# Kernel optimization log

Measured on AMD Instinct MI355X. Metric: run time of the kernel, lower is better.

## Reference

```python
import jax, jax.numpy as jnp
import numpy as np

EPS = 1e-12  # matches torch F.normalize eps


def _l2_normalize(v, axis):
    n = jnp.sqrt(jnp.sum(v * v, axis=axis, keepdims=True))
    return v / jnp.maximum(n, EPS)


def setup_inputs() -> dict:
    key = jax.random.key(0)
    k1, k2 = jax.random.split(key)
    N, D, K = 131072, 512, 64
    x = jax.random.normal(k1, (N, D), dtype=jnp.float32)
    clusters = jax.random.normal(k2, (K, D), dtype=jnp.float32)
    alpha = jnp.ones((), dtype=jnp.float32)
    return {"x": x, "clusters": clusters, "alpha": alpha}


def reference(x, clusters, alpha):
    # cosine similarity between normalized features and normalized codebook
    normed_clusters = _l2_normalize(clusters, axis=1)   # [K, D]
    normed_features = _l2_normalize(x, axis=-1)         # [N, D]
    inner_products = jnp.einsum('nd,kd->nk', normed_features, normed_clusters)  # [N, K]
    # alpha is not None branch: soft assignment
    cluster_probs = jax.nn.softmax(inner_products * alpha, axis=1)  # [N, K]
    cluster_loss = -jnp.mean(jnp.sum(cluster_probs * inner_products, axis=1))
    return cluster_loss, cluster_probs
```

## Files before the change

kernel.cpp:

```cpp
#include <hip/hip_runtime.h>
#include <hip/hip_bf16.h>

#define NROWS 131072
#define DIM   512
#define NK    64

typedef __attribute__((ext_vector_type(4))) float f32x4;
typedef __attribute__((ext_vector_type(8))) short s16x8;

static __device__ __forceinline__ unsigned pk2(float a, float b) {
    union { __hip_bfloat162 h; unsigned u; } cv;
    cv.h = __float22bfloat162_rn(make_float2(a, b));
    return cv.u;
}

__global__ void prep_kernel(const float* __restrict__ cl,
                            unsigned* __restrict__ cb,
                            float* __restrict__ loss_out) {
    const int k = blockIdx.x, t = threadIdx.x;
    const float4* rp = reinterpret_cast<const float4*>(cl + k * DIM);
    float4 f0 = rp[2 * t], f1 = rp[2 * t + 1];
    float ss = f0.x*f0.x + f0.y*f0.y + f0.z*f0.z + f0.w*f0.w
             + f1.x*f1.x + f1.y*f1.y + f1.z*f1.z + f1.w*f1.w;
#pragma unroll
    for (int m = 1; m < 64; m <<= 1) ss += __shfl_xor(ss, m, 64);
    const float rn = 1.0f / fmaxf(sqrtf(ss), 1e-12f);
    uint4 o;
    o.x = pk2(f0.x * rn, f0.y * rn);
    o.y = pk2(f0.z * rn, f0.w * rn);
    o.z = pk2(f1.x * rn, f1.y * rn);
    o.w = pk2(f1.z * rn, f1.w * rn);
    reinterpret_cast<uint4*>(cb + (size_t)k * (DIM / 2))[t] = o;
    if (k == 0 && t == 0) *loss_out = 0.0f;
}

__global__ __launch_bounds__(512, 4) void fused_kernel(
        const float* __restrict__ x,
        const unsigned* __restrict__ cb,
        const float* __restrict__ alphap,
        float* __restrict__ out) {
    __shared__ unsigned short lds[NK * DIM];
    __shared__ float sbuf[8][256];

    for (int u = threadIdx.x; u < NK * DIM / 8; u += blockDim.x) {
        const int r = u >> 6, c6 = u & 63;
        const uint4 v = reinterpret_cast<const uint4*>(cb)[u];
        *reinterpret_cast<uint4*>(&lds[r * DIM + ((c6 ^ (r & 7)) << 3)]) = v;
    }
    __syncthreads();

    const float alpha = alphap[0];
    const int lane = threadIdx.x & 63;
    const int n = lane & 15;
    const int q = lane >> 4;
    const int sw = n & 7;
    const int wid = (int)(threadIdx.x >> 6);
    float* sb = sbuf[wid];
    const int gw = (int)((blockIdx.x * blockDim.x + threadIdx.x) >> 6);
    const int nw = (int)((gridDim.x * blockDim.x) >> 6);

    const unsigned short* b_base = &lds[n * DIM];

    float lossa = 0.0f;

    for (int g = gw; g < NROWS / 16; g += nw) {
        const int row0 = g << 4;
        const float4* xp4 = reinterpret_cast<const float4*>(
            x + (size_t)(row0 + n) * DIM + (q << 3));
        f32x4 a0 = {0.f,0.f,0.f,0.f}, a1 = {0.f,0.f,0.f,0.f};
        f32x4 a2 = {0.f,0.f,0.f,0.f}, a3 = {0.f,0.f,0.f,0.f};
        float ss = 0.0f;

        float4 c0 = xp4[0], c1 = xp4[1];
#pragma unroll
        for (int t = 0; t < 16; t++) {
            float4 d0, d1;
            if (t < 15) { d0 = xp4[(t + 1) * 8]; d1 = xp4[(t + 1) * 8 + 1]; }
            ss += c0.x*c0.x + c0.y*c0.y + c0.z*c0.z + c0.w*c0.w
                + c1.x*c1.x + c1.y*c1.y + c1.z*c1.z + c1.w*c1.w;
            union { s16x8 v; unsigned u[4]; } A;
            A.u[0] = pk2(c0.x, c0.y); A.u[1] = pk2(c0.z, c0.w);
            A.u[2] = pk2(c1.x, c1.y); A.u[3] = pk2(c1.z, c1.w);
            const int off = (((t << 2) | q) ^ sw) << 3;
            const s16x8 b0 = *reinterpret_cast<const s16x8*>(b_base + off);
            const s16x8 b1 = *reinterpret_cast<const s16x8*>(b_base + 16 * DIM + off);
            const s16x8 b2 = *reinterpret_cast<const s16x8*>(b_base + 32 * DIM + off);
            const s16x8 b3 = *reinterpret_cast<const s16x8*>(b_base + 48 * DIM + off);
            a0 = __builtin_amdgcn_mfma_f32_16x16x32_bf16(A.v, b0, a0, 0, 0, 0);
            a1 = __builtin_amdgcn_mfma_f32_16x16x32_bf16(A.v, b1, a1, 0, 0, 0);
            a2 = __builtin_amdgcn_mfma_f32_16x16x32_bf16(A.v, b2, a2, 0, 0, 0);
            a3 = __builtin_amdgcn_mfma_f32_16x16x32_bf16(A.v, b3, a3, 0, 0, 0);
            c0 = d0; c1 = d1;
        }

        ss += __shfl_xor(ss, 16, 64);
        ss += __shfl_xor(ss, 32, 64);
        const float rnorm = 1.0f / fmaxf(sqrtf(ss), 1e-12f);

#pragma unroll
        for (int r = 0; r < 4; r++) {
            const float rn = __shfl(rnorm, (q << 2) + r, 64);
            const float i0 = a0[r] * rn, i1 = a1[r] * rn, i2 = a2[r] * rn, i3 = a3[r] * rn;
            const float z0 = i0 * alpha, z1 = i1 * alpha, z2 = i2 * alpha, z3 = i3 * alpha;
            float mx = fmaxf(fmaxf(z0, z1), fmaxf(z2, z3));
#pragma unroll
            for (int m = 1; m < 16; m <<= 1) mx = fmaxf(mx, __shfl_xor(mx, m, 64));
            const float e0 = __expf(z0 - mx), e1 = __expf(z1 - mx);
            const float e2 = __expf(z2 - mx), e3 = __expf(z3 - mx);
            float s  = e0 + e1 + e2 + e3;
            float sl = e0 * i0 + e1 * i1 + e2 * i2 + e3 * i3;
#pragma unroll
            for (int m = 1; m < 16; m <<= 1) {
                s  += __shfl_xor(s,  m, 64);
                sl += __shfl_xor(sl, m, 64);
            }
            const float inv = 1.0f / s;

            const int qb = q << 6, qs = q << 3;
            sb[qb + (( 0 + n) ^ qs)] = e0 * inv;
            sb[qb + ((16 + n) ^ qs)] = e1 * inv;
            sb[qb + ((32 + n) ^ qs)] = e2 * inv;
            sb[qb + ((48 + n) ^ qs)] = e3 * inv;
            float* gb = out + 1 + (size_t)(row0 + r) * NK;
#pragma unroll
            for (int j = 0; j < 4; j++) {
                const float v = sb[(j << 6) + (lane ^ (j << 3))];
                gb[(size_t)j * 4 * NK + lane] = v;
            }
            if (n == 0) lossa += sl * inv;
        }
    }

    lossa += __shfl_xor(lossa, 16, 64);
    lossa += __shfl_xor(lossa, 32, 64);
    if (lane == 0) atomicAdd(out, -lossa * (1.0f / NROWS));
}

extern "C" void kernel_launch(void* const* d_in, const int* in_sizes, int n_in,
                              void* d_out, int out_size, void* d_ws, size_t ws_size,
                              hipStream_t stream) {
    const float* x  = (const float*)d_in[0];
    const float* cl = (const float*)d_in[1];
    const float* al = (const float*)d_in[2];
    float* out = (float*)d_out;
    unsigned* cb = (unsigned*)d_ws;

    prep_kernel<<<dim3(NK), dim3(64), 0, stream>>>(cl, cb, out);
    fused_kernel<<<dim3(512), dim3(512), 0, stream>>>(x, cb, al, out);
}
```

Measured before the change: 499.8 us.

## Stage full 16-row prob tile in LDS, write aligned rows, deepen prefetch

The per-wave LDS staging buffer grows to hold all 16 output rows, so each row group's probabilities are stored with 16 fully contiguous 256-byte stores. These are offset by one float to account for the leading loss scalar, replacing the four scattered partial-row stores per r. The x load pipeline prefetches two steps ahead instead of one. Launch bounds drop to 2 blocks per CU and the grid halves to 256 blocks, because the larger LDS footprint reduces occupancy. The trade is fewer resident waves and more registers for the deeper prefetch, in exchange for better-coalesced output writes and more load latency hiding.

```diff
diff --git a/kernel.cpp b/kernel.cpp
--- a/kernel.cpp
+++ b/kernel.cpp
@@ -34,18 +34,18 @@
     if (k == 0 && t == 0) *loss_out = 0.0f;
 }
 
-__global__ __launch_bounds__(512, 4) void fused_kernel(
+__global__ __launch_bounds__(512, 2) void fused_kernel(
         const float* __restrict__ x,
         const unsigned* __restrict__ cb,
         const float* __restrict__ alphap,
         float* __restrict__ out) {
-    __shared__ unsigned short lds[NK * DIM];
-    __shared__ float sbuf[8][256];
+    __shared__ unsigned short ldsb[NK * DIM];
+    __shared__ float sbuf[8][1024];
 
     for (int u = threadIdx.x; u < NK * DIM / 8; u += blockDim.x) {
         const int r = u >> 6, c6 = u & 63;
         const uint4 v = reinterpret_cast<const uint4*>(cb)[u];
-        *reinterpret_cast<uint4*>(&lds[r * DIM + ((c6 ^ (r & 7)) << 3)]) = v;
+        *reinterpret_cast<uint4*>(&ldsb[r * DIM + ((c6 ^ (r & 7)) << 3)]) = v;
     }
     __syncthreads();
 
@@ -54,12 +54,11 @@
     const int n = lane & 15;
     const int q = lane >> 4;
     const int sw = n & 7;
-    const int wid = (int)(threadIdx.x >> 6);
-    float* sb = sbuf[wid];
+    float* sb = sbuf[threadIdx.x >> 6];
     const int gw = (int)((blockIdx.x * blockDim.x + threadIdx.x) >> 6);
     const int nw = (int)((gridDim.x * blockDim.x) >> 6);
 
-    const unsigned short* b_base = &lds[n * DIM];
+    const unsigned short* b_base = &ldsb[n * DIM];
 
     float lossa = 0.0f;
 
@@ -72,10 +71,11 @@
         float ss = 0.0f;
 
         float4 c0 = xp4[0], c1 = xp4[1];
+        float4 d0 = xp4[8], d1 = xp4[9];
 #pragma unroll
         for (int t = 0; t < 16; t++) {
-            float4 d0, d1;
-            if (t < 15) { d0 = xp4[(t + 1) * 8]; d1 = xp4[(t + 1) * 8 + 1]; }
+            float4 e0v, e1v;
+            if (t < 14) { e0v = xp4[(t + 2) * 8]; e1v = xp4[(t + 2) * 8 + 1]; }
             ss += c0.x*c0.x + c0.y*c0.y + c0.z*c0.z + c0.w*c0.w
                 + c1.x*c1.x + c1.y*c1.y + c1.z*c1.z + c1.w*c1.w;
             union { s16x8 v; unsigned u[4]; } A;
@@ -90,7 +90,7 @@
             a1 = __builtin_amdgcn_mfma_f32_16x16x32_bf16(A.v, b1, a1, 0, 0, 0);
             a2 = __builtin_amdgcn_mfma_f32_16x16x32_bf16(A.v, b2, a2, 0, 0, 0);
             a3 = __builtin_amdgcn_mfma_f32_16x16x32_bf16(A.v, b3, a3, 0, 0, 0);
-            c0 = d0; c1 = d1;
+            c0 = d0; c1 = d1; d0 = e0v; d1 = e1v;
         }
 
         ss += __shfl_xor(ss, 16, 64);
@@ -115,20 +115,23 @@
                 sl += __shfl_xor(sl, m, 64);
             }
             const float inv = 1.0f / s;
-
-            const int qb = q << 6, qs = q << 3;
-            sb[qb + (( 0 + n) ^ qs)] = e0 * inv;
-            sb[qb + ((16 + n) ^ qs)] = e1 * inv;
-            sb[qb + ((32 + n) ^ qs)] = e2 * inv;
-            sb[qb + ((48 + n) ^ qs)] = e3 * inv;
-            float* gb = out + 1 + (size_t)(row0 + r) * NK;
-#pragma unroll
-            for (int j = 0; j < 4; j++) {
-                const float v = sb[(j << 6) + (lane ^ (j << 3))];
-                gb[(size_t)j * 4 * NK + lane] = v;
-            }
+            float* sr = sb + ((q << 2) + r) * NK;
+            sr[n]      = e0 * inv;
+            sr[n + 16] = e1 * inv;
+            sr[n + 32] = e2 * inv;
+            sr[n + 48] = e3 * inv;
             if (n == 0) lossa += sl * inv;
         }
+
+#pragma unroll
+        for (int k = 0; k < 16; k++) {
+            const int idx = k * 64 + lane - 1;
+            const float v = sb[idx < 0 ? 0 : idx];
+            if (k > 0 || lane > 0)
+                out[(size_t)(row0 + k) * 64 + lane] = v;
+        }
+        if (lane == 0)
+            out[(size_t)(row0 + 16) * 64] = sb[1023];
     }
 
     lossa += __shfl_xor(lossa, 16, 64);
@@ -146,5 +149,5 @@
     unsigned* cb = (unsigned*)d_ws;
 
     prep_kernel<<<dim3(NK), dim3(64), 0, stream>>>(cl, cb, out);
-    fused_kernel<<<dim3(512), dim3(512), 0, stream>>>(x, cb, al, out);
+    fused_kernel<<<dim3(256), dim3(512), 0, stream>>>(x, cb, al, out);
 }
```

New measurement: 412.9 us. 17.4% less time.
